# Optimization experiments

Hardware: AMD Instinct MI355X
Metric: run time of the kernel (lower is better)

The kernel has to match this reference:

```python
import jax, jax.numpy as jnp
import numpy as np

N = 20000
E = 400000
D = 128  # latent_dim


def _bce(p, t):
    # torch F.binary_cross_entropy clamps log terms at -100
    logp = jnp.clip(jnp.log(p), -100.0)
    log1mp = jnp.clip(jnp.log(1.0 - p), -100.0)
    return -jnp.mean(t * logp + (1.0 - t) * log1mp)


def setup_inputs() -> dict:
    key = jax.random.key(0)
    ks = jax.random.split(key, 12)
    pos = jax.random.normal(ks[0], (N,), jnp.float32)
    s = jax.random.uniform(ks[1], (N,), dtype=jnp.float32)
    edge_index = jax.random.randint(ks[2], (2, E), 0, N)
    pi = jax.random.randint(ks[3], (E,), 0, 2)
    pi_h = jax.random.randint(ks[4], (4, E), 0, 2)
    reach_h = jax.random.randint(ks[5], (4, N), 0, 2)
    sc = 0.1
    W_enc = sc * jax.random.normal(ks[6], (2, D), jnp.float32)
    b_enc = jnp.zeros((D,), jnp.float32)
    W_msg = sc * jax.random.normal(ks[7], (2 * D, D), jnp.float32)
    b_msg = jnp.zeros((D,), jnp.float32)
    W_self = sc * jax.random.normal(ks[8], (2 * D, D), jnp.float32)
    W_agg = sc * jax.random.normal(ks[9], (D, D), jnp.float32)
    b_upd = jnp.zeros((D,), jnp.float32)
    W_dec = sc * jax.random.normal(ks[10], (2 * D, 1), jnp.float32)
    b_dec = jnp.zeros((1,), jnp.float32)
    return dict(pos=pos, s=s, edge_index=edge_index, pi=pi, pi_h=pi_h, reach_h=reach_h,
                W_enc=W_enc, b_enc=b_enc, W_msg=W_msg, b_msg=b_msg,
                W_self=W_self, W_agg=W_agg, b_upd=b_upd, W_dec=W_dec, b_dec=b_dec)


def reference(pos, s, edge_index, pi, pi_h, reach_h,
              W_enc, b_enc, W_msg, b_msg, W_self, W_agg, b_upd, W_dec, b_dec):
    n = pos.shape[0]
    src, dst = edge_index[0], edge_index[1]
    idx_both = jnp.concatenate([src, dst])  # incident-edge readout indices
    hints = pi_h[1:].astype(jnp.float32)              # [T, E]
    hints_reach = reach_h[1:].astype(jnp.float32)     # [T, N]
    max_iter = hints.shape[0] + 1

    h = jnp.zeros((n, D), jnp.float32)
    sfeat = s
    preds, preds_y = [], []
    for _ in range(max_iter):  # small fixed iteration count (algorithm steps)
        inp = jnp.stack([pos, sfeat], axis=1)                      # [N, 2]
        z = jax.nn.relu(inp @ W_enc + b_enc)                       # encoder
        x = jnp.concatenate([z, h], axis=1)                        # [N, 2D]
        msg = jax.nn.relu(x[src] @ W_msg + b_msg)                  # [E, D]
        agg = jax.ops.segment_max(msg, dst, num_segments=n)        # scatter-max
        agg = jnp.where(jnp.isfinite(agg), agg, 0.0)
        h = jax.nn.relu(x @ W_self + agg @ W_agg + b_upd)          # processor
        ef = jnp.concatenate([h[src], h[dst]], axis=1)             # [E, 2D]
        alpha = jax.nn.sigmoid(ef @ W_dec + b_dec)[:, 0]           # decoder -> per-edge prob
        preds.append(alpha)
        # per-node max over all incident edges (both endpoints), threshold 0.8
        amax = jax.ops.segment_max(jnp.concatenate([alpha, alpha]), idx_both, num_segments=n)
        y = (amax >= 0.8).astype(jnp.float32)
        preds_y.append(y)
        sfeat = y

    predictions = jnp.stack(preds)        # [max_iter, E]
    predictions_y = jnp.stack(preds_y)    # [max_iter, N]

    loss_x = _bce(predictions[-1], pi.astype(jnp.float32))
    loss_h = jnp.asarray(0.0, jnp.float32)
    for i in range(hints.shape[0]):
        loss_h = loss_h + _bce(predictions[i], hints[i])
    y_loss_x = _bce(predictions_y[-1], reach_h[-1].astype(jnp.float32))
    y_loss_h = jnp.asarray(0.0, jnp.float32)
    for i in range(hints_reach.shape[0]):
        y_loss_h = y_loss_h + _bce(predictions_y[i], hints_reach[i])
    return (y, loss_x, loss_h, y_loss_x, y_loss_h)
```

## Files before the change

kernel.cpp:

```cpp
#include <hip/hip_runtime.h>

#define CSR_B 128

__global__ __launch_bounds__(256) void k_hist2(const int* __restrict__ eidx, int E, int N,
                                               int* __restrict__ partial_d,
                                               int* __restrict__ partial_s) {
  extern __shared__ unsigned int hist[];
  int nw = (N + 1) >> 1;
  for (int i = threadIdx.x; i < 2 * nw; i += blockDim.x) hist[i] = 0u;
  __syncthreads();
  const int* src = eidx;
  const int* dst = eidx + E;
  int chunk = (E + CSR_B - 1) / CSR_B;
  int beg = blockIdx.x * chunk, end = min(E, beg + chunk);
  for (int e = beg + threadIdx.x; e < end; e += blockDim.x) {
    int d = dst[e];
    atomicAdd(&hist[d >> 1], 1u << ((d & 1) * 16));
    int s = src[e];
    atomicAdd(&hist[nw + (s >> 1)], 1u << ((s & 1) * 16));
  }
  __syncthreads();
  for (int i = threadIdx.x; i < N; i += blockDim.x) {
    partial_d[(size_t)blockIdx.x * N + i] = (int)((hist[i >> 1] >> ((i & 1) * 16)) & 0xFFFFu);
    partial_s[(size_t)blockIdx.x * N + i] = (int)((hist[nw + (i >> 1)] >> ((i & 1) * 16)) & 0xFFFFu);
  }
}

__global__ __launch_bounds__(256) void k_colscan2(int* __restrict__ partial_d,
                                                  int* __restrict__ cnt_d,
                                                  int* __restrict__ partial_s,
                                                  int* __restrict__ cnt_s, int N) {
  int g = blockIdx.x * blockDim.x + threadIdx.x;
  int* partial;
  int* cnt;
  int bin;
  if (g < N) { partial = partial_d; cnt = cnt_d; bin = g; }
  else if (g < 2 * N) { partial = partial_s; cnt = cnt_s; bin = g - N; }
  else return;
  int run = 0;
  for (int b = 0; b < CSR_B; ++b) {
    int t = partial[(size_t)b * N + bin];
    partial[(size_t)b * N + bin] = run;
    run += t;
  }
  cnt[bin] = run;
}

__device__ __forceinline__ void scan_one(const int* __restrict__ cnt, int* __restrict__ rp,
                                         int N, int* sums) {
  int t = threadIdx.x;
  int chunk = (N + 1023) / 1024;
  int beg = t * chunk, end = min(N, beg + chunk);
  int s = 0;
  for (int i = beg; i < end; ++i) s += cnt[i];
  sums[t] = s;
  __syncthreads();
  for (int off = 1; off < 1024; off <<= 1) {
    int v = (t >= off) ? sums[t - off] : 0;
    __syncthreads();
    sums[t] += v;
    __syncthreads();
  }
  int run = (t > 0) ? sums[t - 1] : 0;
  if (t == 0) rp[0] = 0;
  for (int i = beg; i < end; ++i) { run += cnt[i]; rp[i + 1] = run; }
}

__global__ __launch_bounds__(1024) void k_scan2both(const int* __restrict__ cnt_d,
                                                    int* __restrict__ rp_d,
                                                    const int* __restrict__ cnt_s,
                                                    int* __restrict__ rp_s, int N) {
  __shared__ int sums[1024];
  scan_one(cnt_d, rp_d, N, sums);
  __syncthreads();
  scan_one(cnt_s, rp_s, N, sums);
}

__global__ __launch_bounds__(256) void k_scatter2(
    const int* __restrict__ eidx, int E, int N,
    const int* __restrict__ partial_d, const int* __restrict__ rp_d, int* __restrict__ csr_src,
    const int* __restrict__ partial_s, const int* __restrict__ rp_s, int* __restrict__ csr_dst) {
  extern __shared__ unsigned int cur[];
  int nw = (N + 1) >> 1;
  for (int i = threadIdx.x; i < 2 * nw; i += blockDim.x) cur[i] = 0u;
  __syncthreads();
  const int* src = eidx;
  const int* dst = eidx + E;
  int chunk = (E + CSR_B - 1) / CSR_B;
  int beg = blockIdx.x * chunk, end = min(E, beg + chunk);
  for (int e = beg + threadIdx.x; e < end; e += blockDim.x) {
    int d = dst[e], s = src[e];
    int shd = (d & 1) * 16;
    unsigned int old = atomicAdd(&cur[d >> 1], 1u << shd);
    csr_src[rp_d[d] + partial_d[(size_t)blockIdx.x * N + d] + (int)((old >> shd) & 0xFFFFu)] = s;
    int shs = (s & 1) * 16;
    unsigned int old2 = atomicAdd(&cur[nw + (s >> 1)], 1u << shs);
    csr_dst[rp_s[s] + partial_s[(size_t)blockIdx.x * N + s] + (int)((old2 >> shs) & 0xFFFFu)] = d;
  }
}

__global__ void k_build_w(const float* __restrict__ W_msg, const float* __restrict__ W_self,
                          const float* __restrict__ b_msg, float* __restrict__ Wcat,
                          float* __restrict__ bcat) {
  int idx = blockIdx.x * blockDim.x + threadIdx.x;
  int k = idx >> 8, j = idx & 255;
  Wcat[idx] = (j < 128) ? W_msg[k * 128 + j] : W_self[k * 128 + (j - 128)];
  if (idx < 256) bcat[idx] = (idx < 128) ? b_msg[idx] : 0.0f;
}

__device__ __forceinline__ float4 enc4(float p, float sf, float4 we0, float4 we1, float4 be) {
  float4 r;
  r.x = fmaxf(fmaf(p, we0.x, fmaf(sf, we1.x, be.x)), 0.f);
  r.y = fmaxf(fmaf(p, we0.y, fmaf(sf, we1.y, be.y)), 0.f);
  r.z = fmaxf(fmaf(p, we0.z, fmaf(sf, we1.z, be.z)), 0.f);
  r.w = fmaxf(fmaf(p, we0.w, fmaf(sf, we1.w, be.w)), 0.f);
  return r;
}

template <bool IT0>
__global__ __launch_bounds__(128) void k_gemm(
    const float* __restrict__ pos, const float* __restrict__ sfeat,
    const float* __restrict__ hsrc, const float* __restrict__ W_enc,
    const float* __restrict__ b_enc, const float* __restrict__ B,
    const float* __restrict__ bias, float* __restrict__ C, int M) {
  __shared__ float As[16][68];
  __shared__ float Bs[16][132];
  const int m0 = blockIdx.x * 64, n0 = blockIdx.y * 128;
  const int t = threadIdx.x;
  const int ty = t >> 4, tx = t & 15;
  const int lr = t >> 1, cq = (t & 1) << 3;
  const int row_ld = m0 + lr;
  const bool valid = row_ld < M;
  float p = 0.f, sf = 0.f;
  if (valid) { p = pos[row_ld]; sf = sfeat[row_ld]; }
  const int bc = (t & 31) << 2, br0 = t >> 5;
  float acc[2][2][4][4] = {};
  const int KMAX = IT0 ? 128 : 256;
  for (int k0 = 0; k0 < KMAX; k0 += 16) {
    const int col = k0 + cq;
    float4 a0 = make_float4(0.f, 0.f, 0.f, 0.f), a1 = a0;
    if (valid) {
      if (col < 128) {
        float4 we0 = *reinterpret_cast<const float4*>(&W_enc[col]);
        float4 we1 = *reinterpret_cast<const float4*>(&W_enc[128 + col]);
        float4 be  = *reinterpret_cast<const float4*>(&b_enc[col]);
        a0 = enc4(p, sf, we0, we1, be);
        we0 = *reinterpret_cast<const float4*>(&W_enc[col + 4]);
        we1 = *reinterpret_cast<const float4*>(&W_enc[128 + col + 4]);
        be  = *reinterpret_cast<const float4*>(&b_enc[col + 4]);
        a1 = enc4(p, sf, we0, we1, be);
      } else {
        a0 = *reinterpret_cast<const float4*>(&hsrc[(size_t)row_ld * 128 + col - 128]);
        a1 = *reinterpret_cast<const float4*>(&hsrc[(size_t)row_ld * 128 + col - 124]);
      }
    }
    As[cq + 0][lr] = a0.x; As[cq + 1][lr] = a0.y;
    As[cq + 2][lr] = a0.z; As[cq + 3][lr] = a0.w;
    As[cq + 4][lr] = a1.x; As[cq + 5][lr] = a1.y;
    As[cq + 6][lr] = a1.z; As[cq + 7][lr] = a1.w;
#pragma unroll
    for (int pp = 0; pp < 4; ++pp) {
      int br = br0 + pp * 4;
      *reinterpret_cast<float4*>(&Bs[br][bc]) =
          *reinterpret_cast<const float4*>(&B[(size_t)(k0 + br) * 256 + n0 + bc]);
    }
    __syncthreads();
#pragma unroll
    for (int k = 0; k < 16; ++k) {
      float4 alo = *reinterpret_cast<const float4*>(&As[k][ty * 4]);
      float4 ahi = *reinterpret_cast<const float4*>(&As[k][32 + ty * 4]);
      float4 blo = *reinterpret_cast<const float4*>(&Bs[k][tx * 4]);
      float4 bhi = *reinterpret_cast<const float4*>(&Bs[k][64 + tx * 4]);
      const float av[2][4] = {{alo.x, alo.y, alo.z, alo.w}, {ahi.x, ahi.y, ahi.z, ahi.w}};
      const float bv[2][4] = {{blo.x, blo.y, blo.z, blo.w}, {bhi.x, bhi.y, bhi.z, bhi.w}};
#pragma unroll
      for (int ih = 0; ih < 2; ++ih)
#pragma unroll
        for (int jh = 0; jh < 2; ++jh)
#pragma unroll
          for (int i = 0; i < 4; ++i)
#pragma unroll
            for (int j = 0; j < 4; ++j)
              acc[ih][jh][i][j] = fmaf(av[ih][i], bv[jh][j], acc[ih][jh][i][j]);
    }
    __syncthreads();
  }
#pragma unroll
  for (int jh = 0; jh < 2; ++jh) {
    const int colb = n0 + jh * 64 + tx * 4;
    float4 b4 = *reinterpret_cast<const float4*>(&bias[colb]);
#pragma unroll
    for (int ih = 0; ih < 2; ++ih)
#pragma unroll
      for (int i = 0; i < 4; ++i) {
        int row = m0 + ih * 32 + ty * 4 + i;
        if (row < M) {
          float4 o = make_float4(acc[ih][jh][i][0] + b4.x, acc[ih][jh][i][1] + b4.y,
                                 acc[ih][jh][i][2] + b4.z, acc[ih][jh][i][3] + b4.w);
          *reinterpret_cast<float4*>(&C[(size_t)row * 256 + colb]) = o;
        }
      }
  }
}

__global__ __launch_bounds__(256) void k_aggmax(
    const float* __restrict__ xw, const int* __restrict__ row_ptr,
    const int* __restrict__ csr_src, float* __restrict__ agg, int N, int Nh) {
  const int cx = blockIdx.x & 7;
  const int chunk = cx & 3;
  const int half = cx >> 2;
  const int hw = threadIdx.x >> 5;
  const int sub = threadIdx.x & 31;
  const int node = half * Nh + blockIdx.y * 8 + hw;
  const int hi = half ? N : Nh;
  if (node >= hi) return;
  const float* base = xw + chunk * 32 + sub;
  const int beg = row_ptr[node], end = row_ptr[node + 1];
  float m0 = 0.f, m1 = 0.f, m2 = 0.f, m3 = 0.f;
  int i = beg;
  for (; i + 3 < end; i += 4) {
    int e0 = csr_src[i], e1 = csr_src[i + 1], e2 = csr_src[i + 2], e3 = csr_src[i + 3];
    float f0 = base[(size_t)e0 * 256];
    float f1 = base[(size_t)e1 * 256];
    float f2 = base[(size_t)e2 * 256];
    float f3 = base[(size_t)e3 * 256];
    m0 = fmaxf(m0, f0); m1 = fmaxf(m1, f1);
    m2 = fmaxf(m2, f2); m3 = fmaxf(m3, f3);
  }
  for (; i < end; ++i) m0 = fmaxf(m0, base[(size_t)csr_src[i] * 256]);
  m0 = fmaxf(fmaxf(m0, m1), fmaxf(m2, m3));
  agg[(size_t)node * 128 + chunk * 32 + sub] = m0;
}

__global__ __launch_bounds__(256) void k_update2(
    const float* __restrict__ agg, const float* __restrict__ W_agg,
    const float* __restrict__ b_upd, const float* __restrict__ xw,
    const float* __restrict__ W_dec, const float* __restrict__ b_dec,
    float* __restrict__ h, float* __restrict__ u, float* __restrict__ v, int M) {
  __shared__ float As[32][33];
  __shared__ float Bs[32][128];
  const int m0 = blockIdx.x * 32;
  const int t = threadIdx.x;
  const int ty = t >> 5, tx = t & 31;
  const int lar = t >> 3, lac = (t & 7) << 2;
  float acc[4][4] = {};
  for (int k0 = 0; k0 < 128; k0 += 32) {
    {
      float4 av = make_float4(0.f, 0.f, 0.f, 0.f);
      int row = m0 + lar;
      if (row < M) av = *reinterpret_cast<const float4*>(&agg[(size_t)row * 128 + k0 + lac]);
      As[lar][lac + 0] = av.x;
      As[lar][lac + 1] = av.y;
      As[lar][lac + 2] = av.z;
      As[lar][lac + 3] = av.w;
#pragma unroll
      for (int p = 0; p < 4; ++p) {
        int br = (t >> 5) + p * 8;
        *reinterpret_cast<float4*>(&Bs[br][tx * 4]) =
            *reinterpret_cast<const float4*>(&W_agg[(size_t)(k0 + br) * 128 + tx * 4]);
      }
    }
    __syncthreads();
#pragma unroll
    for (int k = 0; k < 32; ++k) {
      float4 b4 = *reinterpret_cast<const float4*>(&Bs[k][tx * 4]);
      const float bb[4] = {b4.x, b4.y, b4.z, b4.w};
#pragma unroll
      for (int j = 0; j < 4; ++j) {
        float a = As[ty * 4 + j][k];
#pragma unroll
        for (int c = 0; c < 4; ++c) acc[j][c] = fmaf(a, bb[c], acc[j][c]);
      }
    }
    __syncthreads();
  }
  const float4 bu4 = *reinterpret_cast<const float4*>(&b_upd[tx * 4]);
  const float4 wdu = *reinterpret_cast<const float4*>(&W_dec[tx * 4]);
  const float4 wdv = *reinterpret_cast<const float4*>(&W_dec[128 + tx * 4]);
  const float bd = b_dec[0];
#pragma unroll
  for (int j = 0; j < 4; ++j) {
    int row = m0 + ty * 4 + j;
    if (row >= M) continue;
    float4 sf = *reinterpret_cast<const float4*>(&xw[(size_t)row * 256 + 128 + tx * 4]);
    float4 h4;
    h4.x = fmaxf(acc[j][0] + sf.x + bu4.x, 0.f);
    h4.y = fmaxf(acc[j][1] + sf.y + bu4.y, 0.f);
    h4.z = fmaxf(acc[j][2] + sf.z + bu4.z, 0.f);
    h4.w = fmaxf(acc[j][3] + sf.w + bu4.w, 0.f);
    *reinterpret_cast<float4*>(&h[(size_t)row * 128 + tx * 4]) = h4;
    float up = h4.x * wdu.x + h4.y * wdu.y + h4.z * wdu.z + h4.w * wdu.w;
    float vp = h4.x * wdv.x + h4.y * wdv.y + h4.z * wdv.z + h4.w * wdv.w;
#pragma unroll
    for (int m = 16; m > 0; m >>= 1) {
      up += __shfl_xor(up, m);
      vp += __shfl_xor(vp, m);
    }
    if (tx == 0) {
      u[row] = up + bd;
      v[row] = vp;
    }
  }
}

#define GB 512
__global__ __launch_bounds__(256) void k_losses(
    const int* __restrict__ src, const int* __restrict__ dst, const float* __restrict__ u,
    const float* __restrict__ v, const int* __restrict__ tgt, const int* __restrict__ row_ptr,
    const int* __restrict__ csr_src, const int* __restrict__ row_ptr2,
    const int* __restrict__ csr_dst, const int* __restrict__ reach_row,
    float* __restrict__ ybuf, float* __restrict__ yout, int write_out,
    double* __restrict__ pe_slot, double* __restrict__ py_slot, int E, int N) {
  __shared__ double wsum[4];
  double term = 0.0;
  for (int e = blockIdx.x * blockDim.x + threadIdx.x; e < E; e += GB * 256) {
    float l = u[src[e]] + v[dst[e]];
    float a = 1.0f / (1.0f + expf(-l));
    float t = (float)tgt[e];
    float lp = fmaxf(logf(a), -100.0f);
    float l1 = fmaxf(logf(1.0f - a), -100.0f);
    term += (double)(t * lp + (1.0f - t) * l1);
  }
#pragma unroll
  for (int off = 32; off > 0; off >>= 1) term += __shfl_down(term, off);
  if ((threadIdx.x & 63) == 0) wsum[threadIdx.x >> 6] = term;
  __syncthreads();
  if (threadIdx.x == 0) pe_slot[blockIdx.x] = wsum[0] + wsum[1] + wsum[2] + wsum[3];
  __syncthreads();
  double c = 0.0;
  for (int n = blockIdx.x * blockDim.x + threadIdx.x; n < N; n += GB * 256) {
    float mu = -INFINITY, mv = -INFINITY;
    const int b1 = row_ptr[n], e1 = row_ptr[n + 1];
    for (int i = b1; i < e1; ++i) mu = fmaxf(mu, u[csr_src[i]]);
    const int b2 = row_ptr2[n], e2 = row_ptr2[n + 1];
    for (int i = b2; i < e2; ++i) mv = fmaxf(mv, v[csr_dst[i]]);
    float m = fmaxf(mu + v[n], u[n] + mv);
    float a = 1.0f / (1.0f + expf(-m));
    float yv = (a >= 0.8f) ? 1.0f : 0.0f;
    ybuf[n] = yv;
    if (write_out) yout[n] = yv;
    if ((float)reach_row[n] != yv) c = 100.0;
  }
#pragma unroll
  for (int off = 32; off > 0; off >>= 1) c += __shfl_down(c, off);
  if ((threadIdx.x & 63) == 0) wsum[threadIdx.x >> 6] = c;
  __syncthreads();
  if (threadIdx.x == 0) py_slot[blockIdx.x] = wsum[0] + wsum[1] + wsum[2] + wsum[3];
}

__global__ void k_final(const double* __restrict__ pe, const double* __restrict__ py,
                        float* __restrict__ out4, int N, int E, int T) {
  __shared__ double le[8], ly[8];
  int lane = threadIdx.x;
  for (int it = 0; it < T; ++it) {
    double s = 0.0;
    for (int i = lane; i < GB; i += 64) s += pe[(size_t)it * GB + i];
#pragma unroll
    for (int off = 32; off > 0; off >>= 1) s += __shfl_down(s, off);
    if (lane == 0) le[it] = s;
    double s2 = 0.0;
    for (int i = lane; i < GB; i += 64) s2 += py[(size_t)it * GB + i];
#pragma unroll
    for (int off = 32; off > 0; off >>= 1) s2 += __shfl_down(s2, off);
    if (lane == 0) ly[it] = s2;
  }
  __syncthreads();
  if (lane == 0) {
    float loss_x = (float)(-le[T - 1] / (double)E);
    float loss_h = 0.0f;
    for (int i = 0; i < T - 1; ++i) loss_h += (float)(-le[i] / (double)E);
    float yl_x = (float)(ly[T - 1] / (double)N);
    float yl_h = 0.0f;
    for (int i = 0; i < T - 1; ++i) yl_h += (float)(ly[i] / (double)N);
    out4[0] = loss_x;
    out4[1] = loss_h;
    out4[2] = yl_x;
    out4[3] = yl_h;
  }
}

extern "C" void kernel_launch(void* const* d_in, const int* in_sizes, int n_in,
                              void* d_out, int out_size, void* d_ws, size_t ws_size,
                              hipStream_t stream) {
  const float* pos = (const float*)d_in[0];
  const float* s = (const float*)d_in[1];
  const int* eidx = (const int*)d_in[2];
  const int* pi = (const int*)d_in[3];
  const int* pi_h = (const int*)d_in[4];
  const int* reach = (const int*)d_in[5];
  const float* W_enc = (const float*)d_in[6];
  const float* b_enc = (const float*)d_in[7];
  const float* W_msg = (const float*)d_in[8];
  const float* b_msg = (const float*)d_in[9];
  const float* W_self = (const float*)d_in[10];
  const float* W_agg = (const float*)d_in[11];
  const float* b_upd = (const float*)d_in[12];
  const float* W_dec = (const float*)d_in[13];
  const float* b_dec = (const float*)d_in[14];

  const int N = in_sizes[0];
  const int E = in_sizes[3];
  const int T = in_sizes[4] / in_sizes[3];
  const int* src = eidx;
  const int* dst = eidx + E;

  char* w = (char*)d_ws;
  auto alloc = [&](size_t bytes) {
    char* p = w;
    w += (bytes + 255) & ~(size_t)255;
    return p;
  };
  float* xw = (float*)alloc((size_t)N * 256 * 4);
  float* agg = (float*)alloc((size_t)N * 128 * 4);
  float* h = (float*)alloc((size_t)N * 128 * 4);
  float* Wcat = (float*)alloc(256 * 256 * 4);
  float* bcat = (float*)alloc(256 * 4);
  float* u = (float*)alloc((size_t)N * 4);
  float* v = (float*)alloc((size_t)N * 4);
  float* ybuf = (float*)alloc((size_t)N * 4);
  int* cnt_d = (int*)alloc((size_t)N * 4);
  int* cnt_s = (int*)alloc((size_t)N * 4);
  int* row_ptr = (int*)alloc((size_t)(N + 1) * 4);
  int* row_ptr2 = (int*)alloc((size_t)(N + 1) * 4);
  int* csr_src = (int*)alloc((size_t)E * 4);
  int* csr_dst = (int*)alloc((size_t)E * 4);
  int* partial_d = (int*)alloc((size_t)CSR_B * N * 4);
  int* partial_s = (int*)alloc((size_t)CSR_B * N * 4);
  double* pe = (double*)alloc((size_t)T * GB * 8);
  double* py = (double*)alloc((size_t)T * GB * 8);

  float* outy = (float*)d_out;
  float* out4 = outy + N;

  k_build_w<<<256, 256, 0, stream>>>(W_msg, W_self, b_msg, Wcat, bcat);

  const size_t lds2 = (size_t)2 * ((N + 1) >> 1) * 4;
  k_hist2<<<CSR_B, 256, lds2, stream>>>(eidx, E, N, partial_d, partial_s);
  k_colscan2<<<(2 * N + 255) / 256, 256, 0, stream>>>(partial_d, cnt_d, partial_s, cnt_s, N);
  k_scan2both<<<1, 1024, 0, stream>>>(cnt_d, row_ptr, cnt_s, row_ptr2, N);
  k_scatter2<<<CSR_B, 256, lds2, stream>>>(eidx, E, N, partial_d, row_ptr, csr_src, partial_s,
                                           row_ptr2, csr_dst);

  const int Nh = (N + 1) / 2;
  const int NB = (Nh + 7) / 8;

  const float* sfeat = s;
  for (int it = 0; it < T; ++it) {
    dim3 g1((N + 63) / 64, 2);
    if (it == 0)
      k_gemm<true><<<g1, 128, 0, stream>>>(pos, sfeat, h, W_enc, b_enc, Wcat, bcat, xw, N);
    else
      k_gemm<false><<<g1, 128, 0, stream>>>(pos, sfeat, h, W_enc, b_enc, Wcat, bcat, xw, N);

    k_aggmax<<<dim3(8, NB), 256, 0, stream>>>(xw, row_ptr, csr_src, agg, N, Nh);

    k_update2<<<(N + 31) / 32, 256, 0, stream>>>(agg, W_agg, b_upd, xw, W_dec, b_dec,
                                                 h, u, v, N);

    const int* tgt = (it < T - 1) ? (pi_h + (size_t)(it + 1) * E) : pi;
    const int* rrow = (it < T - 1) ? (reach + (size_t)(it + 1) * N) : (reach + (size_t)(T - 1) * N);
    k_losses<<<GB, 256, 0, stream>>>(src, dst, u, v, tgt, row_ptr, csr_src, row_ptr2, csr_dst,
                                     rrow, ybuf, outy, (it == T - 1) ? 1 : 0,
                                     pe + (size_t)it * GB, py + (size_t)it * GB, E, N);
    sfeat = ybuf;
  }
  k_final<<<1, 64, 0, stream>>>(pe, py, out4, N, E, T);
}
```

Before: 574.2 us.

## Split-K the node GEMM into two partial buffers plus reduction kernel

```diff
diff --git a/kernel.cpp b/kernel.cpp
--- a/kernel.cpp
+++ b/kernel.cpp
@@ -1,6 +1,6 @@
 #include <hip/hip_runtime.h>
 
-#define CSR_B 128
+#define CSR_B 64
 
 __global__ __launch_bounds__(256) void k_hist2(const int* __restrict__ eidx, int E, int N,
                                                int* __restrict__ partial_d,
@@ -122,57 +122,67 @@
     const float* __restrict__ pos, const float* __restrict__ sfeat,
     const float* __restrict__ hsrc, const float* __restrict__ W_enc,
     const float* __restrict__ b_enc, const float* __restrict__ B,
-    const float* __restrict__ bias, float* __restrict__ C, int M) {
-  __shared__ float As[16][68];
-  __shared__ float Bs[16][132];
-  const int m0 = blockIdx.x * 64, n0 = blockIdx.y * 128;
+    float* __restrict__ Cpart, int M) {
+  __shared__ float As[16][132];
+  __shared__ float Bs[16][68];
+  const int KH = IT0 ? 64 : 128;
+  const int kbase = blockIdx.z * KH;
+  const bool ENCB = (kbase < 128);
+  const int m0 = blockIdx.x * 128, n0 = blockIdx.y * 64;
   const int t = threadIdx.x;
-  const int ty = t >> 4, tx = t & 15;
-  const int lr = t >> 1, cq = (t & 1) << 3;
-  const int row_ld = m0 + lr;
-  const bool valid = row_ld < M;
-  float p = 0.f, sf = 0.f;
-  if (valid) { p = pos[row_ld]; sf = sfeat[row_ld]; }
-  const int bc = (t & 31) << 2, br0 = t >> 5;
+  const int ty = t >> 3;
+  const int tx = t & 7;
+  const int ar = t >> 2, acq = (t & 3) << 2;
+  float pv[4], sv[4];
+  if (ENCB) {
+#pragma unroll
+    for (int p = 0; p < 4; ++p) {
+      int r = m0 + p * 32 + ar;
+      pv[p] = (r < M) ? pos[r] : 0.f;
+      sv[p] = (r < M) ? sfeat[r] : 0.f;
+    }
+  }
+  const int br0 = t >> 4, bc4 = (t & 15) << 2;
   float acc[2][2][4][4] = {};
-  const int KMAX = IT0 ? 128 : 256;
-  for (int k0 = 0; k0 < KMAX; k0 += 16) {
-    const int col = k0 + cq;
-    float4 a0 = make_float4(0.f, 0.f, 0.f, 0.f), a1 = a0;
-    if (valid) {
-      if (col < 128) {
-        float4 we0 = *reinterpret_cast<const float4*>(&W_enc[col]);
-        float4 we1 = *reinterpret_cast<const float4*>(&W_enc[128 + col]);
-        float4 be  = *reinterpret_cast<const float4*>(&b_enc[col]);
-        a0 = enc4(p, sf, we0, we1, be);
-        we0 = *reinterpret_cast<const float4*>(&W_enc[col + 4]);
-        we1 = *reinterpret_cast<const float4*>(&W_enc[128 + col + 4]);
-        be  = *reinterpret_cast<const float4*>(&b_enc[col + 4]);
-        a1 = enc4(p, sf, we0, we1, be);
-      } else {
-        a0 = *reinterpret_cast<const float4*>(&hsrc[(size_t)row_ld * 128 + col - 128]);
-        a1 = *reinterpret_cast<const float4*>(&hsrc[(size_t)row_ld * 128 + col - 124]);
+  for (int k0 = kbase; k0 < kbase + KH; k0 += 16) {
+    const int col = k0 + acq;
+    if (ENCB) {
+      float4 we0 = *reinterpret_cast<const float4*>(&W_enc[col]);
+      float4 we1 = *reinterpret_cast<const float4*>(&W_enc[128 + col]);
+      float4 be  = *reinterpret_cast<const float4*>(&b_enc[col]);
+#pragma unroll
+      for (int p = 0; p < 4; ++p) {
+        float4 av = enc4(pv[p], sv[p], we0, we1, be);
+        int row = p * 32 + ar;
+        As[acq + 0][row] = av.x; As[acq + 1][row] = av.y;
+        As[acq + 2][row] = av.z; As[acq + 3][row] = av.w;
       }
-    }
-    As[cq + 0][lr] = a0.x; As[cq + 1][lr] = a0.y;
-    As[cq + 2][lr] = a0.z; As[cq + 3][lr] = a0.w;
-    As[cq + 4][lr] = a1.x; As[cq + 5][lr] = a1.y;
-    As[cq + 6][lr] = a1.z; As[cq + 7][lr] = a1.w;
-#pragma unroll
-    for (int pp = 0; pp < 4; ++pp) {
-      int br = br0 + pp * 4;
-      *reinterpret_cast<float4*>(&Bs[br][bc]) =
-          *reinterpret_cast<const float4*>(&B[(size_t)(k0 + br) * 256 + n0 + bc]);
+    } else {
+#pragma unroll
+      for (int p = 0; p < 4; ++p) {
+        int row = p * 32 + ar;
+        int r = m0 + row;
+        float4 av = make_float4(0.f, 0.f, 0.f, 0.f);
+        if (r < M) av = *reinterpret_cast<const float4*>(&hsrc[(size_t)r * 128 + col - 128]);
+        As[acq + 0][row] = av.x; As[acq + 1][row] = av.y;
+        As[acq + 2][row] = av.z; As[acq + 3][row] = av.w;
+      }
+    }
+#pragma unroll
+    for (int q = 0; q < 2; ++q) {
+      int brow = q * 8 + br0;
+      *reinterpret_cast<float4*>(&Bs[brow][bc4]) =
+          *reinterpret_cast<const float4*>(&B[(size_t)(k0 + brow) * 256 + n0 + bc4]);
     }
     __syncthreads();
 #pragma unroll
     for (int k = 0; k < 16; ++k) {
-      float4 alo = *reinterpret_cast<const float4*>(&As[k][ty * 4]);
-      float4 ahi = *reinterpret_cast<const float4*>(&As[k][32 + ty * 4]);
-      float4 blo = *reinterpret_cast<const float4*>(&Bs[k][tx * 4]);
-      float4 bhi = *reinterpret_cast<const float4*>(&Bs[k][64 + tx * 4]);
-      const float av[2][4] = {{alo.x, alo.y, alo.z, alo.w}, {ahi.x, ahi.y, ahi.z, ahi.w}};
-      const float bv[2][4] = {{blo.x, blo.y, blo.z, blo.w}, {bhi.x, bhi.y, bhi.z, bhi.w}};
+      float4 a0 = *reinterpret_cast<const float4*>(&As[k][ty * 4]);
+      float4 a1 = *reinterpret_cast<const float4*>(&As[k][64 + ty * 4]);
+      float4 b0 = *reinterpret_cast<const float4*>(&Bs[k][tx * 4]);
+      float4 b1 = *reinterpret_cast<const float4*>(&Bs[k][32 + tx * 4]);
+      const float av[2][4] = {{a0.x, a0.y, a0.z, a0.w}, {a1.x, a1.y, a1.z, a1.w}};
+      const float bv[2][4] = {{b0.x, b0.y, b0.z, b0.w}, {b1.x, b1.y, b1.z, b1.w}};
 #pragma unroll
       for (int ih = 0; ih < 2; ++ih)
 #pragma unroll
@@ -185,22 +195,33 @@
     }
     __syncthreads();
   }
-#pragma unroll
-  for (int jh = 0; jh < 2; ++jh) {
-    const int colb = n0 + jh * 64 + tx * 4;
-    float4 b4 = *reinterpret_cast<const float4*>(&bias[colb]);
-#pragma unroll
-    for (int ih = 0; ih < 2; ++ih)
-#pragma unroll
-      for (int i = 0; i < 4; ++i) {
-        int row = m0 + ih * 32 + ty * 4 + i;
-        if (row < M) {
-          float4 o = make_float4(acc[ih][jh][i][0] + b4.x, acc[ih][jh][i][1] + b4.y,
-                                 acc[ih][jh][i][2] + b4.z, acc[ih][jh][i][3] + b4.w);
-          *reinterpret_cast<float4*>(&C[(size_t)row * 256 + colb]) = o;
-        }
+  float* dstp = Cpart + (size_t)blockIdx.z * M * 256;
+#pragma unroll
+  for (int ih = 0; ih < 2; ++ih)
+#pragma unroll
+    for (int i = 0; i < 4; ++i) {
+      int row = m0 + ih * 64 + ty * 4 + i;
+      if (row >= M) continue;
+#pragma unroll
+      for (int jh = 0; jh < 2; ++jh) {
+        float4 o = make_float4(acc[ih][jh][i][0], acc[ih][jh][i][1],
+                               acc[ih][jh][i][2], acc[ih][jh][i][3]);
+        *reinterpret_cast<float4*>(&dstp[(size_t)row * 256 + n0 + jh * 32 + tx * 4]) = o;
       }
-  }
+    }
+}
+
+__global__ __launch_bounds__(256) void k_addc(const float* __restrict__ Cpart,
+                                              const float* __restrict__ bias,
+                                              float* __restrict__ xw, int M) {
+  int gid = blockIdx.x * blockDim.x + threadIdx.x;
+  int n = gid >> 6, q = (gid & 63) << 2;
+  if (n >= M) return;
+  float4 a = *reinterpret_cast<const float4*>(&Cpart[(size_t)n * 256 + q]);
+  float4 b = *reinterpret_cast<const float4*>(&Cpart[(size_t)(M + n) * 256 + q]);
+  float4 c = *reinterpret_cast<const float4*>(&bias[q]);
+  a.x += b.x + c.x; a.y += b.y + c.y; a.z += b.z + c.z; a.w += b.w + c.w;
+  *reinterpret_cast<float4*>(&xw[(size_t)n * 256 + q]) = a;
 }
 
 __global__ __launch_bounds__(256) void k_aggmax(
@@ -237,7 +258,7 @@
     const float* __restrict__ b_upd, const float* __restrict__ xw,
     const float* __restrict__ W_dec, const float* __restrict__ b_dec,
     float* __restrict__ h, float* __restrict__ u, float* __restrict__ v, int M) {
-  __shared__ float As[32][33];
+  __shared__ float AsT[32][33];
   __shared__ float Bs[32][128];
   const int m0 = blockIdx.x * 32;
   const int t = threadIdx.x;
@@ -249,10 +270,10 @@
       float4 av = make_float4(0.f, 0.f, 0.f, 0.f);
       int row = m0 + lar;
       if (row < M) av = *reinterpret_cast<const float4*>(&agg[(size_t)row * 128 + k0 + lac]);
-      As[lar][lac + 0] = av.x;
-      As[lar][lac + 1] = av.y;
-      As[lar][lac + 2] = av.z;
-      As[lar][lac + 3] = av.w;
+      AsT[lac + 0][lar] = av.x;
+      AsT[lac + 1][lar] = av.y;
+      AsT[lac + 2][lar] = av.z;
+      AsT[lac + 3][lar] = av.w;
 #pragma unroll
       for (int p = 0; p < 4; ++p) {
         int br = (t >> 5) + p * 8;
@@ -263,14 +284,14 @@
     __syncthreads();
 #pragma unroll
     for (int k = 0; k < 32; ++k) {
+      float4 a4 = *reinterpret_cast<const float4*>(&AsT[k][ty * 4]);
       float4 b4 = *reinterpret_cast<const float4*>(&Bs[k][tx * 4]);
+      const float aa[4] = {a4.x, a4.y, a4.z, a4.w};
       const float bb[4] = {b4.x, b4.y, b4.z, b4.w};
 #pragma unroll
-      for (int j = 0; j < 4; ++j) {
-        float a = As[ty * 4 + j][k];
-#pragma unroll
-        for (int c = 0; c < 4; ++c) acc[j][c] = fmaf(a, bb[c], acc[j][c]);
-      }
+      for (int j = 0; j < 4; ++j)
+#pragma unroll
+        for (int c = 0; c < 4; ++c) acc[j][c] = fmaf(aa[j], bb[c], acc[j][c]);
     }
     __syncthreads();
   }
@@ -410,6 +431,9 @@
     w += (bytes + 255) & ~(size_t)255;
     return p;
   };
+  float* Cpart = (float*)alloc((size_t)2 * N * 256 * 4);
+  int* partial_d = (int*)Cpart;
+  int* partial_s = partial_d + (size_t)CSR_B * N;
   float* xw = (float*)alloc((size_t)N * 256 * 4);
   float* agg = (float*)alloc((size_t)N * 128 * 4);
   float* h = (float*)alloc((size_t)N * 128 * 4);
@@ -424,8 +448,6 @@
   int* row_ptr2 = (int*)alloc((size_t)(N + 1) * 4);
   int* csr_src = (int*)alloc((size_t)E * 4);
   int* csr_dst = (int*)alloc((size_t)E * 4);
-  int* partial_d = (int*)alloc((size_t)CSR_B * N * 4);
-  int* partial_s = (int*)alloc((size_t)CSR_B * N * 4);
   double* pe = (double*)alloc((size_t)T * GB * 8);
   double* py = (double*)alloc((size_t)T * GB * 8);
 
@@ -446,11 +468,13 @@
 
   const float* sfeat = s;
   for (int it = 0; it < T; ++it) {
-    dim3 g1((N + 63) / 64, 2);
+    dim3 g1((N + 127) / 128, 4, 2);
     if (it == 0)
-      k_gemm<true><<<g1, 128, 0, stream>>>(pos, sfeat, h, W_enc, b_enc, Wcat, bcat, xw, N);
+      k_gemm<true><<<g1, 128, 0, stream>>>(pos, sfeat, h, W_enc, b_enc, Wcat, Cpart, N);
     else
-      k_gemm<false><<<g1, 128, 0, stream>>>(pos, sfeat, h, W_enc, b_enc, Wcat, bcat, xw, N);
+      k_gemm<false><<<g1, 128, 0, stream>>>(pos, sfeat, h, W_enc, b_enc, Wcat, Cpart, N);
+
+    k_addc<<<(N * 64 + 255) / 256, 256, 0, stream>>>(Cpart, bcat, xw, N);
 
     k_aggmax<<<dim3(8, NB), 256, 0, stream>>>(xw, row_ptr, csr_src, agg, N, Nh);
 
```

Result: slower. 612.1 us (+6.6%).
